# Kernel tuning notes

Measured on AMD Instinct MI355X. Metric: run time of the kernel, lower is better.

Reference implementation:

```python
import jax, jax.numpy as jnp
import numpy as np

MARGIN = 0.3
PD_EPS = 1e-6  # torch F.pairwise_distance adds eps to the difference


def setup_inputs() -> dict:
    key = jax.random.key(0)
    k1, k2 = jax.random.split(key)
    B, D, NUM_CLASSES = 8192, 256, 8
    embeddings = jax.random.normal(k1, (B, D), dtype=jnp.float32)
    labels = jax.random.randint(k2, (B,), 0, NUM_CLASSES, dtype=jnp.int64)
    return {"embeddings": embeddings, "labels": labels}


def _pairwise_euclidean(x):
    # cdist(x, x, p=2) via the Gram trick; clamp tiny negatives before sqrt
    sq = jnp.sum(x * x, axis=1)  # [B]
    d2 = sq[:, None] + sq[None, :] - 2.0 * (x @ x.T)
    return jnp.sqrt(jnp.maximum(d2, 0.0))


def reference(embeddings, labels):
    B = embeddings.shape[0]
    D = _pairwise_euclidean(embeddings)  # [B, B]

    eq = labels[:, None] == labels[None, :]
    eye = jnp.eye(B, dtype=bool)
    pos_mask = eq & ~eye          # same label, not self
    neg_mask = ~eq                # different label

    # hard mining: per anchor, farthest positive and closest negative
    pos_idx = jnp.argmax(jnp.where(pos_mask, D, -jnp.inf), axis=1)  # [B]
    neg_idx = jnp.argmin(jnp.where(neg_mask, D, jnp.inf), axis=1)   # [B]
    valid = pos_mask.any(axis=1) & neg_mask.any(axis=1)             # [B]

    # recompute triplet distances like F.pairwise_distance (eps on the diff)
    pos_dist = jnp.linalg.norm(embeddings - embeddings[pos_idx] + PD_EPS, axis=1)
    neg_dist = jnp.linalg.norm(embeddings - embeddings[neg_idx] + PD_EPS, axis=1)

    per_anchor = jax.nn.relu(pos_dist - neg_dist + MARGIN)
    n_valid = jnp.maximum(valid.sum(), 1)
    loss = jnp.sum(jnp.where(valid, per_anchor, 0.0)) / n_valid.astype(per_anchor.dtype)
    return loss
```

## Files before the change

### kernel.cpp

```cpp
#include <hip/hip_runtime.h>
#include <math.h>


typedef __attribute__((ext_vector_type(8))) short short8;
typedef __attribute__((ext_vector_type(4))) float floatx4;

#define B_N 8192
#define D_K 256

__device__ __forceinline__ unsigned short f2bf_rne(float f) {
  unsigned u = __float_as_uint(f);
  u += 0x7FFFu + ((u >> 16) & 1u);
  return (unsigned short)(u >> 16);
}

__global__ void k_split(const float* __restrict__ x, unsigned short* __restrict__ xhf,
                        float* __restrict__ sqq,
                        float* __restrict__ sum, int* __restrict__ cnt,
                        int* __restrict__ done) {
  __shared__ float sw[64];
  const int tid  = threadIdx.x;
  const int lane = tid & 63;
  const int w    = tid >> 6;
  const int b    = blockIdx.x;
  const int m    = lane & 15;
  const int quad = lane >> 4;
  const int row  = b * 16 + m;

  float s = 0.f;
#pragma unroll
  for (int h = 0; h < 2; ++h) {
    int tk = w + h * 4;
    int kk = tk * 32 + quad * 8;
    float4 f0 = *reinterpret_cast<const float4*>(x + (size_t)row * D_K + kk);
    float4 f1 = *reinterpret_cast<const float4*>(x + (size_t)row * D_K + kk + 4);
    s += f0.x * f0.x + f0.y * f0.y + f0.z * f0.z + f0.w * f0.w;
    s += f1.x * f1.x + f1.y * f1.y + f1.z * f1.z + f1.w * f1.w;
    ushort4 lo, hi;
    lo.x = f2bf_rne(f0.x); lo.y = f2bf_rne(f0.y); lo.z = f2bf_rne(f0.z); lo.w = f2bf_rne(f0.w);
    hi.x = f2bf_rne(f1.x); hi.y = f2bf_rne(f1.y); hi.z = f2bf_rne(f1.z); hi.w = f2bf_rne(f1.w);
    size_t o = ((size_t)b * 8 + tk) * 512 + lane * 8;
    *reinterpret_cast<ushort4*>(xhf + o)     = lo;
    *reinterpret_cast<ushort4*>(xhf + o + 4) = hi;
  }
  s += __shfl_xor(s, 16);
  s += __shfl_xor(s, 32);
  if (quad == 0) sw[w * 16 + m] = s;
  __syncthreads();
  if (tid < 16) {
    int i = b * 16 + tid;
    float t = sw[tid] + sw[16 + tid] + sw[32 + tid] + sw[48 + tid];
    sqq[i] = fmaf(t, 128.f, 262144.f);
  }
  if (b == 0 && tid == 0) { *sum = 0.f; *cnt = 0; *done = 0; }
}

__global__ __launch_bounds__(512) void k_mine16(
    const unsigned short* __restrict__ xhf, const int* __restrict__ lab,
    const float* __restrict__ sqq,
    unsigned* __restrict__ ppart, unsigned* __restrict__ npart) {
  __shared__ unsigned short Alds[8 * 8 * 512];
  __shared__ unsigned jbp[8 * 64], jbn[8 * 64];

  int t  = blockIdx.x;
  int bi = (int)(64.5f - sqrtf(64.5f * 64.5f - 2.f * (float)t));
  int b0 = 64 * bi - (bi * (bi - 1)) / 2;
  if (t < b0) { bi--; b0 = 64 * bi - (bi * (bi - 1)) / 2; }
  else {
    int b1 = 64 * (bi + 1) - ((bi + 1) * bi) / 2;
    if (t >= b1) { bi++; b0 = b1; }
  }
  const int bj = bi + (t - b0);

  const int tid  = threadIdx.x;
  const int lane = tid & 63;
  const int w    = tid >> 6;
  const int wi   = w >> 1;
  const int wj   = w & 1;
  const int quad = lane >> 4, l15 = lane & 15;
  const int i0   = bi * 128;

  {
    const short8* src = reinterpret_cast<const short8*>(xhf + (size_t)bi * 32768);
    short8* dst = reinterpret_cast<short8*>(Alds);
#pragma unroll
    for (int it = 0; it < 8; ++it) dst[it * 512 + tid] = src[it * 512 + tid];
  }

  unsigned pkey[8], nkey[8];
  unsigned lip = 0;
  float    sqi[8];
#pragma unroll
  for (int r = 0; r < 8; ++r) {
    pkey[r] = 0u; nkey[r] = 0xFFFFFFFFu;
    int ir = i0 + wi * 32 + (r >> 2) * 16 + quad * 4 + (r & 3);
    lip |= ((unsigned)lab[ir] & 0xFu) << (r * 4);
    sqi[r] = sqq[ir];
  }
  __syncthreads();

  const unsigned short* Bw = xhf + ((size_t)(bj * 8 + wj * 4) * 8) * 512 + lane * 8;
  const unsigned short* Aw = Alds + (size_t)(wi * 2) * 8 * 512 + lane * 8;

  floatx4 acc[8];
#pragma unroll
  for (int q = 0; q < 8; ++q) acc[q] = (floatx4)0.f;

#pragma unroll
  for (int tk = 0; tk < 8; ++tk) {
    short8 Bf[4];
#pragma unroll
    for (int nt = 0; nt < 4; ++nt)
      Bf[nt] = *reinterpret_cast<const short8*>(Bw + nt * 4096 + tk * 512);
    short8 Af[2];
#pragma unroll
    for (int mt = 0; mt < 2; ++mt)
      Af[mt] = *reinterpret_cast<const short8*>(Aw + (size_t)(mt * 8 + tk) * 512);
#pragma unroll
    for (int mt = 0; mt < 2; ++mt)
#pragma unroll
      for (int nt = 0; nt < 4; ++nt)
        acc[mt * 4 + nt] = __builtin_amdgcn_mfma_f32_16x16x32_bf16(
            Af[mt], Bf[nt], acc[mt * 4 + nt], 0, 0, 0);
  }

#pragma unroll
  for (int nt = 0; nt < 4; ++nt) {
    int      j  = bj * 128 + wj * 64 + nt * 16 + l15;
    unsigned jl = (unsigned)lab[j] & 0xFu;
    float    sj = sqq[j];
    unsigned jp = 0u, jn = 0xFFFFFFFFu;
#pragma unroll
    for (int r = 0; r < 8; ++r) {
      float dot = acc[(r >> 2) * 4 + nt][r & 3];
      int   ir  = i0 + wi * 32 + (r >> 2) * 16 + quad * 4 + (r & 3);
      bool  eq  = (jl == ((lip >> (r * 4)) & 0xFu));
      unsigned kqi  = (unsigned)fmaf(-256.f, dot, sj);
      unsigned keyi = (kqi << 13) | (unsigned)j;
      unsigned pci = eq ? keyi : 0u;
      unsigned nci = eq ? 0xFFFFFFFFu : keyi;
      pkey[r] = pkey[r] > pci ? pkey[r] : pci;
      nkey[r] = nkey[r] < nci ? nkey[r] : nci;
      unsigned kqj  = (unsigned)fmaf(-256.f, dot, sqi[r]);
      unsigned keyj = (kqj << 13) | (unsigned)ir;
      unsigned pcj = eq ? keyj : 0u;
      unsigned ncj = eq ? 0xFFFFFFFFu : keyj;
      jp = jp > pcj ? jp : pcj;
      jn = jn < ncj ? jn : ncj;
    }
#pragma unroll
    for (int m = 16; m < 64; m <<= 1) {
      unsigned op = (unsigned)__shfl_xor((int)jp, m);
      unsigned on = (unsigned)__shfl_xor((int)jn, m);
      jp = jp > op ? jp : op;
      jn = jn < on ? jn : on;
    }
    if (quad == 0) {
      jbp[w * 64 + nt * 16 + l15] = jp;
      jbn[w * 64 + nt * 16 + l15] = jn;
    }
  }

#pragma unroll
  for (int r = 0; r < 8; ++r) {
    unsigned p = pkey[r], n = nkey[r];
#pragma unroll
    for (int m = 1; m < 16; m <<= 1) {
      unsigned op = (unsigned)__shfl_xor((int)p, m);
      unsigned on = (unsigned)__shfl_xor((int)n, m);
      p = p > op ? p : op;
      n = n < on ? n : on;
    }
    if (l15 == 0) {
      int ir = i0 + wi * 32 + (r >> 2) * 16 + quad * 4 + (r & 3);
      size_t idx = (size_t)(2 * bj + wj) * B_N + ir;
      ppart[idx] = p;
      npart[idx] = n;
    }
  }

  __syncthreads();
  if ((wi & 1) == 0 && bi != bj) {
    unsigned p = jbp[w * 64 + lane];
    unsigned n = jbn[w * 64 + lane];
    unsigned p2 = jbp[(w ^ 2) * 64 + lane];
    unsigned n2 = jbn[(w ^ 2) * 64 + lane];
    p = p > p2 ? p : p2;
    n = n < n2 ? n : n2;
    int j = bj * 128 + wj * 64 + lane;
    size_t idx = (size_t)(2 * bi + (wi >> 1)) * B_N + j;
    ppart[idx] = p;
    npart[idx] = n;
  }
}

__global__ void k_finish(const float* __restrict__ x,
                         const unsigned* __restrict__ ppart,
                         const unsigned* __restrict__ npart,
                         float* __restrict__ sum, int* __restrict__ cnt,
                         int* __restrict__ done, float* __restrict__ out) {
  __shared__ unsigned spk[32], snk[32];
  __shared__ float ssum[4];
  __shared__ int   scnt[4];
  const int tid = threadIdx.x;
  const int a0  = blockIdx.x * 32;

  if (tid < 32) { spk[tid] = 0u; snk[tid] = 0xFFFFFFFFu; }
  __syncthreads();

  {
    const int a    = a0 + (tid & 31);
    const int part = tid >> 5;
    unsigned p = 0u, n = 0xFFFFFFFFu;
#pragma unroll
    for (int s = 0; s < 16; ++s) {
      size_t idx = (size_t)(part * 16 + s) * B_N + a;
      unsigned pv = ppart[idx];
      unsigned nv = npart[idx];
      p = p > pv ? p : pv;
      n = n < nv ? n : nv;
    }
    atomicMax(&spk[tid & 31], p);
    atomicMin(&snk[tid & 31], n);
  }
  __syncthreads();

  const int w = tid >> 6, lane = tid & 63;
  float lsum = 0.f; int lcnt = 0;
#pragma unroll
  for (int it = 0; it < 8; ++it) {
    int al = w * 8 + it;
    int a  = a0 + al;
    unsigned p = spk[al];
    unsigned n = snk[al];
    bool valid = (p != 0u) && (n != 0xFFFFFFFFu);
    int  pidx = valid ? (int)(p & 8191u) : 0;
    int  nidx = valid ? (int)(n & 8191u) : 0;

    float4 xa = *reinterpret_cast<const float4*>(x + (size_t)a * D_K + lane * 4);
    float4 xp = *reinterpret_cast<const float4*>(x + (size_t)pidx * D_K + lane * 4);
    float4 xn = *reinterpret_cast<const float4*>(x + (size_t)nidx * D_K + lane * 4);
    float dx, sp = 0.f, sn = 0.f;
    dx = xa.x - xp.x + 1e-6f; sp = fmaf(dx, dx, sp);
    dx = xa.y - xp.y + 1e-6f; sp = fmaf(dx, dx, sp);
    dx = xa.z - xp.z + 1e-6f; sp = fmaf(dx, dx, sp);
    dx = xa.w - xp.w + 1e-6f; sp = fmaf(dx, dx, sp);
    dx = xa.x - xn.x + 1e-6f; sn = fmaf(dx, dx, sn);
    dx = xa.y - xn.y + 1e-6f; sn = fmaf(dx, dx, sn);
    dx = xa.z - xn.z + 1e-6f; sn = fmaf(dx, dx, sn);
    dx = xa.w - xn.w + 1e-6f; sn = fmaf(dx, dx, sn);
#pragma unroll
    for (int o = 32; o > 0; o >>= 1) {
      sp += __shfl_down(sp, o, 64);
      sn += __shfl_down(sn, o, 64);
    }
    if (lane == 0 && valid) {
      float per = sqrtf(sp) - sqrtf(sn) + 0.3f;
      if (per > 0.f) lsum += per;
      lcnt += 1;
    }
  }
  if (lane == 0) { ssum[w] = lsum; scnt[w] = lcnt; }
  __syncthreads();
  if (tid == 0) {
    atomicAdd(sum, ssum[0] + ssum[1] + ssum[2] + ssum[3]);
    atomicAdd(cnt, scnt[0] + scnt[1] + scnt[2] + scnt[3]);
    __threadfence();
    int prev = atomicAdd(done, 1);
    if (prev == gridDim.x - 1) {
      float s = atomicAdd(sum, 0.f);
      int   cc = atomicAdd(cnt, 0);
      if (cc < 1) cc = 1;
      out[0] = s / (float)cc;
    }
  }
}

extern "C" void kernel_launch(void* const* d_in, const int* in_sizes, int n_in,
                              void* d_out, int out_size, void* d_ws, size_t ws_size,
                              hipStream_t stream) {
  const float* x   = (const float*)d_in[0];
  const int*   lab = (const int*)d_in[1];
  float*       out = (float*)d_out;

  char* ws = (char*)d_ws;
  unsigned short* xhf = (unsigned short*)ws;
  float* sqq = (float*)(ws + (size_t)4608 * 1024);
  char*  pb = ws + (size_t)4608 * 1024 + 65536;
  size_t seg = (size_t)128 * B_N * 4;
  unsigned* ppart = (unsigned*)(pb);
  unsigned* npart = (unsigned*)(pb + seg);
  float* sum  = (float*)(pb + 2 * seg);
  int*   cnt  = (int*)(sum + 1);
  int*   done = (int*)(sum + 2);

  k_split<<<B_N / 16, 256, 0, stream>>>(x, xhf, sqq, sum, cnt, done);
  k_mine16<<<2080, 512, 0, stream>>>(xhf, lab, sqq, ppart, npart);
  k_finish<<<B_N / 32, 256, 0, stream>>>(x, ppart, npart, sum, cnt, done, out);
}
```

Baseline: 123.0 us.

## Split mining blocks in half, drop LDS A-staging, use DPP row reductions

```diff
diff --git a/kernel.cpp b/kernel.cpp
--- a/kernel.cpp
+++ b/kernel.cpp
@@ -13,6 +13,9 @@
   u += 0x7FFFu + ((u >> 16) & 1u);
   return (unsigned short)(u >> 16);
 }
+
+#define DPP_SHR(x, CTRL) \
+  ((unsigned)__builtin_amdgcn_update_dpp((int)(x), (int)(x), (CTRL), 0xF, 0xF, false))
 
 __global__ void k_split(const float* __restrict__ x, unsigned short* __restrict__ xhf,
                         float* __restrict__ sqq,
@@ -55,14 +58,15 @@
   if (b == 0 && tid == 0) { *sum = 0.f; *cnt = 0; *done = 0; }
 }
 
-__global__ __launch_bounds__(512) void k_mine16(
+__global__ __launch_bounds__(256, 6) void k_mine16(
     const unsigned short* __restrict__ xhf, const int* __restrict__ lab,
     const float* __restrict__ sqq,
     unsigned* __restrict__ ppart, unsigned* __restrict__ npart) {
-  __shared__ unsigned short Alds[8 * 8 * 512];
-  __shared__ unsigned jbp[8 * 64], jbn[8 * 64];
+  __shared__ unsigned jbp[4 * 64], jbn[4 * 64];
 
   int t  = blockIdx.x;
+  const int hb = t & 1;
+  t >>= 1;
   int bi = (int)(64.5f - sqrtf(64.5f * 64.5f - 2.f * (float)t));
   int b0 = 64 * bi - (bi * (bi - 1)) / 2;
   if (t < b0) { bi--; b0 = 64 * bi - (bi * (bi - 1)) / 2; }
@@ -78,29 +82,19 @@
   const int wi   = w >> 1;
   const int wj   = w & 1;
   const int quad = lane >> 4, l15 = lane & 15;
-  const int i0   = bi * 128;
-
-  {
-    const short8* src = reinterpret_cast<const short8*>(xhf + (size_t)bi * 32768);
-    short8* dst = reinterpret_cast<short8*>(Alds);
-#pragma unroll
-    for (int it = 0; it < 8; ++it) dst[it * 512 + tid] = src[it * 512 + tid];
-  }
-
-  unsigned pkey[8], nkey[8];
+  const int i0   = bi * 128 + hb * 64 + wi * 32;
+
   unsigned lip = 0;
   float    sqi[8];
 #pragma unroll
   for (int r = 0; r < 8; ++r) {
-    pkey[r] = 0u; nkey[r] = 0xFFFFFFFFu;
-    int ir = i0 + wi * 32 + (r >> 2) * 16 + quad * 4 + (r & 3);
+    int ir = i0 + (r >> 2) * 16 + quad * 4 + (r & 3);
     lip |= ((unsigned)lab[ir] & 0xFu) << (r * 4);
     sqi[r] = sqq[ir];
   }
-  __syncthreads();
-
-  const unsigned short* Bw = xhf + ((size_t)(bj * 8 + wj * 4) * 8) * 512 + lane * 8;
-  const unsigned short* Aw = Alds + (size_t)(wi * 2) * 8 * 512 + lane * 8;
+
+  const unsigned aoff = (unsigned)(i0 >> 4) * 4096u + (unsigned)lane * 8u;
+  const unsigned boff = (unsigned)(bj * 8 + wj * 4) * 4096u + (unsigned)lane * 8u;
 
   floatx4 acc[8];
 #pragma unroll
@@ -111,11 +105,11 @@
     short8 Bf[4];
 #pragma unroll
     for (int nt = 0; nt < 4; ++nt)
-      Bf[nt] = *reinterpret_cast<const short8*>(Bw + nt * 4096 + tk * 512);
+      Bf[nt] = *reinterpret_cast<const short8*>(xhf + boff + (unsigned)(nt * 4096 + tk * 512));
     short8 Af[2];
 #pragma unroll
     for (int mt = 0; mt < 2; ++mt)
-      Af[mt] = *reinterpret_cast<const short8*>(Aw + (size_t)(mt * 8 + tk) * 512);
+      Af[mt] = *reinterpret_cast<const short8*>(xhf + aoff + (unsigned)(mt * 4096 + tk * 512));
 #pragma unroll
     for (int mt = 0; mt < 2; ++mt)
 #pragma unroll
@@ -123,6 +117,10 @@
         acc[mt * 4 + nt] = __builtin_amdgcn_mfma_f32_16x16x32_bf16(
             Af[mt], Bf[nt], acc[mt * 4 + nt], 0, 0, 0);
   }
+
+  unsigned pkey[8], nkey[8];
+#pragma unroll
+  for (int r = 0; r < 8; ++r) { pkey[r] = 0u; nkey[r] = 0xFFFFFFFFu; }
 
 #pragma unroll
   for (int nt = 0; nt < 4; ++nt) {
@@ -133,7 +131,7 @@
 #pragma unroll
     for (int r = 0; r < 8; ++r) {
       float dot = acc[(r >> 2) * 4 + nt][r & 3];
-      int   ir  = i0 + wi * 32 + (r >> 2) * 16 + quad * 4 + (r & 3);
+      int   ir  = i0 + (r >> 2) * 16 + quad * 4 + (r & 3);
       bool  eq  = (jl == ((lip >> (r * 4)) & 0xFu));
       unsigned kqi  = (unsigned)fmaf(-256.f, dot, sj);
       unsigned keyi = (kqi << 13) | (unsigned)j;
@@ -163,32 +161,44 @@
 
 #pragma unroll
   for (int r = 0; r < 8; ++r) {
-    unsigned p = pkey[r], n = nkey[r];
-#pragma unroll
-    for (int m = 1; m < 16; m <<= 1) {
-      unsigned op = (unsigned)__shfl_xor((int)p, m);
-      unsigned on = (unsigned)__shfl_xor((int)n, m);
-      p = p > op ? p : op;
-      n = n < on ? n : on;
-    }
-    if (l15 == 0) {
-      int ir = i0 + wi * 32 + (r >> 2) * 16 + quad * 4 + (r & 3);
+    unsigned tp = DPP_SHR(pkey[r], 0x118); pkey[r] = pkey[r] > tp ? pkey[r] : tp;
+    unsigned tn = DPP_SHR(nkey[r], 0x118); nkey[r] = nkey[r] < tn ? nkey[r] : tn;
+  }
+#pragma unroll
+  for (int r = 0; r < 8; ++r) {
+    unsigned tp = DPP_SHR(pkey[r], 0x114); pkey[r] = pkey[r] > tp ? pkey[r] : tp;
+    unsigned tn = DPP_SHR(nkey[r], 0x114); nkey[r] = nkey[r] < tn ? nkey[r] : tn;
+  }
+#pragma unroll
+  for (int r = 0; r < 8; ++r) {
+    unsigned tp = DPP_SHR(pkey[r], 0x112); pkey[r] = pkey[r] > tp ? pkey[r] : tp;
+    unsigned tn = DPP_SHR(nkey[r], 0x112); nkey[r] = nkey[r] < tn ? nkey[r] : tn;
+  }
+#pragma unroll
+  for (int r = 0; r < 8; ++r) {
+    unsigned tp = DPP_SHR(pkey[r], 0x111); pkey[r] = pkey[r] > tp ? pkey[r] : tp;
+    unsigned tn = DPP_SHR(nkey[r], 0x111); nkey[r] = nkey[r] < tn ? nkey[r] : tn;
+  }
+#pragma unroll
+  for (int r = 0; r < 8; ++r) {
+    if (l15 == 15) {
+      int ir = i0 + (r >> 2) * 16 + quad * 4 + (r & 3);
       size_t idx = (size_t)(2 * bj + wj) * B_N + ir;
-      ppart[idx] = p;
-      npart[idx] = n;
-    }
-  }
-
-  __syncthreads();
-  if ((wi & 1) == 0 && bi != bj) {
-    unsigned p = jbp[w * 64 + lane];
-    unsigned n = jbn[w * 64 + lane];
-    unsigned p2 = jbp[(w ^ 2) * 64 + lane];
-    unsigned n2 = jbn[(w ^ 2) * 64 + lane];
+      ppart[idx] = pkey[r];
+      npart[idx] = nkey[r];
+    }
+  }
+
+  __syncthreads();
+  if (wi == 0 && bi != bj) {
+    unsigned p  = jbp[w * 64 + lane];
+    unsigned n  = jbn[w * 64 + lane];
+    unsigned p2 = jbp[(w + 2) * 64 + lane];
+    unsigned n2 = jbn[(w + 2) * 64 + lane];
     p = p > p2 ? p : p2;
     n = n < n2 ? n : n2;
     int j = bj * 128 + wj * 64 + lane;
-    size_t idx = (size_t)(2 * bi + (wi >> 1)) * B_N + j;
+    size_t idx = (size_t)(2 * bi + hb) * B_N + j;
     ppart[idx] = p;
     npart[idx] = n;
   }
@@ -295,6 +305,6 @@
   int*   done = (int*)(sum + 2);
 
   k_split<<<B_N / 16, 256, 0, stream>>>(x, xhf, sqq, sum, cnt, done);
-  k_mine16<<<2080, 512, 0, stream>>>(xhf, lab, sqq, ppart, npart);
+  k_mine16<<<4160, 256, 0, stream>>>(xhf, lab, sqq, ppart, npart);
   k_finish<<<B_N / 32, 256, 0, stream>>>(x, ppart, npart, sum, cnt, done, out);
 }
```

Result: no change. 121.8 us (-1.0%).
